# Kernel optimization log

Measured on AMD Instinct MI355X. Metric: run time of the kernel, lower is better.

Reference implementation:

```python
import jax, jax.numpy as jnp
import numpy as np

HIDDEN = 768
NUM_HEADS = 8
NUM_CELLS = 16384
MAX_HDRS = 8
NUM_HEADERS = 512
LN_EPS = 1e-5


def setup_inputs() -> dict:
    key = jax.random.key(0)
    ks = jax.random.split(key, 16)
    s = 0.02
    D = HIDDEN
    return {
        "cell_value_embeddings": jax.random.normal(ks[0], (NUM_CELLS, D), jnp.float32),
        "header_embeddings": jax.random.normal(ks[1], (NUM_HEADERS, D), jnp.float32),
        "cell_to_header_map": jax.random.randint(ks[2], (NUM_CELLS, MAX_HDRS), 0, NUM_HEADERS),
        "cell_positions": jax.random.randint(ks[3], (NUM_CELLS, 2), 0, 100),
        # nn.MultiheadAttention params
        "in_proj_w": jax.random.normal(ks[4], (3 * D, D), jnp.float32) * s,
        "in_proj_b": jnp.zeros((3 * D,), jnp.float32),
        "out_w": jax.random.normal(ks[5], (D, D), jnp.float32) * s,
        "out_b": jnp.zeros((D,), jnp.float32),
        # positional embedding tables
        "row_emb": jax.random.normal(ks[6], (100, D), jnp.float32) * s,
        "col_emb": jax.random.normal(ks[7], (100, D), jnp.float32) * s,
        # fusion: Linear(2D->D) + LayerNorm
        "fus_w": jax.random.normal(ks[8], (D, 2 * D), jnp.float32) * s,
        "fus_b": jnp.zeros((D,), jnp.float32),
        "ln_g": jnp.ones((D,), jnp.float32),
        "ln_b": jnp.zeros((D,), jnp.float32),
    }


def _forward(cell_value_embeddings, header_embeddings, in_proj_w, in_proj_b,
             out_w, out_b, row_emb, col_emb, fus_w, fus_b, ln_g, ln_b,
             cell_to_header_map, cell_positions):
    N, D = cell_value_embeddings.shape
    H = cell_to_header_map.shape[1]
    nh, dh = NUM_HEADS, D // NUM_HEADS
    scale = 1.0 / (dh ** 0.5)

    pos = jnp.clip(cell_positions, 0, 99)
    cwp = cell_value_embeddings + row_emb[pos[:, 0]] + col_emb[pos[:, 1]]  # [N,D]

    ids = cell_to_header_map
    mask = ids >= 0                                   # [N,H] valid header slots
    hg = header_embeddings[jnp.where(mask, ids, 0)]   # [N,H,D] gathered K/V inputs

    Wq, Wk, Wv = jnp.split(in_proj_w, 3, axis=0)
    bq, bk, bv = jnp.split(in_proj_b, 3)
    q = (cwp @ Wq.T + bq).reshape(N, nh, dh)          # [N,a,d]
    k = (hg @ Wk.T + bk).reshape(N, H, nh, dh)        # [N,k,a,d]
    v = (hg @ Wv.T + bv).reshape(N, H, nh, dh)

    scores = jnp.einsum('nad,nkad->nak', q, k) * scale          # [N,a,k]
    scores = jnp.where(mask[:, None, :], scores, -1e9)
    attn = jax.nn.softmax(scores, axis=-1)
    attn = jnp.where(mask[:, None, :], attn, 0.0)
    ctx = jnp.einsum('nak,nkad->nad', attn, v).reshape(N, D)
    att_out = ctx @ out_w.T + out_b                    # [N,D]

    comb = jnp.concatenate([cwp, att_out], axis=-1)    # [N,2D]
    h = comb @ fus_w.T + fus_b
    mu = jnp.mean(h, axis=-1, keepdims=True)
    var = jnp.mean((h - mu) ** 2, axis=-1, keepdims=True)
    h = (h - mu) * jax.lax.rsqrt(var + LN_EPS) * ln_g + ln_b
    fused = jax.nn.relu(h)

    has = jnp.any(mask, axis=-1)                       # cells with >=1 valid header
    enriched = jnp.where(has[:, None], fused, cwp)
    weights = jnp.where(mask, attn.mean(axis=1), 0.0)  # head-averaged attn [N,H]
    return enriched, weights


def reference(cell_value_embeddings, header_embeddings, cell_to_header_map,
              cell_positions, in_proj_w, in_proj_b, out_w, out_b, row_emb,
              col_emb, fus_w, fus_b, ln_g, ln_b):
    return _forward(cell_value_embeddings, header_embeddings, in_proj_w,
                    in_proj_b, out_w, out_b, row_emb, col_emb, fus_w, fus_b,
                    ln_g, ln_b, cell_to_header_map, cell_positions)
```

## Files before the change

### kernel.cpp

```cpp
#include <hip/hip_runtime.h>
#include <hip/hip_bf16.h>

#define NCELLS 16384
#define DIM    768
#define NHEADS 8
#define DHEAD  96
#define MAXH   8
#define ND     (NCELLS * DIM)


using bf16 = __hip_bfloat16;
typedef short  short8  __attribute__((ext_vector_type(8)));
typedef short  short4v __attribute__((ext_vector_type(4)));
typedef float  floatx4 __attribute__((ext_vector_type(4)));

__device__ inline short f2b(float f) {
    bf16 h = __float2bfloat16(f);
    unsigned short u; __builtin_memcpy(&u, &h, 2); return (short)u;
}
__device__ inline float b2f(short u) {
    unsigned x = ((unsigned)(unsigned short)u) << 16;
    float f; __builtin_memcpy(&f, &x, 4); return f;
}

__device__ inline short8 ld8(const float* p) {
    floatx4 a = *reinterpret_cast<const floatx4*>(p);
    floatx4 b = *reinterpret_cast<const floatx4*>(p + 4);
    short8 o;
#pragma unroll
    for (int i = 0; i < 4; ++i) { o[i] = f2b(a[i]); o[i + 4] = f2b(b[i]); }
    return o;
}

__device__ __forceinline__ void cp16(const void* g, void* l) {
    __builtin_amdgcn_global_load_lds(
        (const __attribute__((address_space(1))) void*)g,
        (__attribute__((address_space(3))) void*)l, 16, 0, 0);
}

template <int DUAL, int COUT>
__global__ __launch_bounds__(256) void gemm_bf(
    const bf16* __restrict__ A, const bf16* __restrict__ A2,
    const bf16* __restrict__ W, int ldw,
    const float* __restrict__ bias,
    float* __restrict__ Cf, bf16* __restrict__ Cb, int K)
{
    __shared__ short As[128 * 64];
    __shared__ short Bs[128 * 64];
    const int tid = threadIdx.x, wave = tid >> 6, lane = tid & 63;
    const int id = blockIdx.x;
    const int m0 = (id & 127) * 128;
    const int n0 = (id >> 7) * 128;
    const int wr = (wave & 1) * 64, wc = (wave >> 1) * 64;
    const int fr = lane & 15, kg = lane >> 4;

    const int srow = lane >> 3;
    const int scol = (lane & 7) ^ srow;

    floatx4 acc[16];
#pragma unroll
    for (int i = 0; i < 16; ++i) acc[i] = (floatx4){0.f, 0.f, 0.f, 0.f};

    for (int k0 = 0; k0 < K; k0 += 64) {
        const bf16* Ak; int ka;
        if (!DUAL || k0 < DIM) { Ak = A;  ka = k0; }
        else                   { Ak = A2; ka = k0 - DIM; }

        __syncthreads();
#pragma unroll
        for (int i = 0; i < 4; ++i) {
            const int c = i * 4 + wave;
            const int row = c * 8 + srow;
            cp16(Ak + (size_t)(m0 + row) * DIM + ka + scol * 8,
                 &As[c * 512 + lane * 8]);
            cp16(W  + (size_t)(n0 + row) * ldw + k0 + scol * 8,
                 &Bs[c * 512 + lane * 8]);
        }
        __syncthreads();

#pragma unroll
        for (int kk = 0; kk < 2; ++kk) {
            short8 af[4], bfv[4];
#pragma unroll
            for (int i = 0; i < 4; ++i) {
                const int sa = ((kk * 4 + kg) ^ (fr & 7)) * 8;
                af[i]  = *reinterpret_cast<const short8*>(&As[(wr + i * 16 + fr) * 64 + sa]);
                bfv[i] = *reinterpret_cast<const short8*>(&Bs[(wc + i * 16 + fr) * 64 + sa]);
            }
#pragma unroll
            for (int i = 0; i < 4; ++i)
#pragma unroll
                for (int j = 0; j < 4; ++j)
                    acc[i * 4 + j] = __builtin_amdgcn_mfma_f32_16x16x32_bf16(
                        af[i], bfv[j], acc[i * 4 + j], 0, 0, 0);
        }
    }

    const int col_l = lane & 15, row_q = kg * 4;
#pragma unroll
    for (int j = 0; j < 4; ++j) {
        const int col = n0 + wc + j * 16 + col_l;
        const float bv = bias[col];
#pragma unroll
        for (int i = 0; i < 4; ++i) {
#pragma unroll
            for (int r = 0; r < 4; ++r) {
                const int row = m0 + wr + i * 16 + row_q + r;
                const float v = acc[i * 4 + j][r] + bv;
                if (COUT == 0) Cf[(size_t)row * DIM + col] = v;
                else           Cb[(size_t)row * DIM + col] = __float2bfloat16(v);
            }
        }
    }
}

__global__ __launch_bounds__(256) void prep_kernel(
    const float* __restrict__ ce, const int* __restrict__ pos,
    const float* __restrict__ re, const float* __restrict__ co,
    bf16* __restrict__ cwp_b,
    const float* __restrict__ in_proj_w, bf16* __restrict__ Wq_b,
    const float* __restrict__ fus_w,     bf16* __restrict__ Wf_b,
    const float* __restrict__ out_w, const float* __restrict__ out_b,
    const float* __restrict__ fus_b, float* __restrict__ bco,
    const float* __restrict__ hdr, const float* __restrict__ in_proj_b,
    bf16* __restrict__ HKV)
{
    __shared__ short As[64 * 72];
    __shared__ short Bs[64 * 72];
    const int b = blockIdx.x, tid = threadIdx.x;

    if (b < 192) {
        const int m0 = (b & 7) * 64, n0 = (b >> 3) * 64;
        const float* W = in_proj_w + (size_t)DIM * DIM;
        const float* bias = in_proj_b + DIM;
        const int wave = tid >> 6, lane = tid & 63;
        const int lr = tid >> 2, lc = (tid & 3) * 16;
        const int fr = lane & 15, fk = (lane >> 4) * 8;

        floatx4 acc[4];
#pragma unroll
        for (int i = 0; i < 4; ++i) acc[i] = (floatx4){0.f, 0.f, 0.f, 0.f};

        const float* ap = hdr + (size_t)(m0 + lr) * DIM + lc;
        const float* wp = W   + (size_t)(n0 + lr) * DIM + lc;
        short8 a0 = ld8(ap), a1 = ld8(ap + 8);
        short8 w0 = ld8(wp), w1 = ld8(wp + 8);

        for (int it = 0; it < 12; ++it) {
            __syncthreads();
            *reinterpret_cast<short8*>(&As[lr * 72 + lc])     = a0;
            *reinterpret_cast<short8*>(&As[lr * 72 + lc + 8]) = a1;
            *reinterpret_cast<short8*>(&Bs[lr * 72 + lc])     = w0;
            *reinterpret_cast<short8*>(&Bs[lr * 72 + lc + 8]) = w1;
            __syncthreads();
            if (it < 11) {
                const int k0 = (it + 1) * 64;
                a0 = ld8(ap + k0); a1 = ld8(ap + k0 + 8);
                w0 = ld8(wp + k0); w1 = ld8(wp + k0 + 8);
            }
#pragma unroll
            for (int kk = 0; kk < 2; ++kk) {
                short8 af = *reinterpret_cast<const short8*>(
                    &As[(wave * 16 + fr) * 72 + kk * 32 + fk]);
#pragma unroll
                for (int t = 0; t < 4; ++t) {
                    short8 bfv = *reinterpret_cast<const short8*>(
                        &Bs[(t * 16 + fr) * 72 + kk * 32 + fk]);
                    acc[t] = __builtin_amdgcn_mfma_f32_16x16x32_bf16(af, bfv, acc[t], 0, 0, 0);
                }
            }
        }
        const int col_l = lane & 15, row_q = (lane >> 4) * 4;
#pragma unroll
        for (int t = 0; t < 4; ++t) {
            const int col = n0 + t * 16 + col_l;
            const float bv = bias[col];
#pragma unroll
            for (int r = 0; r < 4; ++r) {
                const int row = m0 + wave * 16 + row_q + r;
                HKV[(size_t)row * 1536 + col] = __float2bfloat16(acc[t][r] + bv);
            }
        }
    } else if (b < 336) {
        const int b3 = b - 192;
        const int n0  = (b3 % 12) * 64;
        const int k0t = (b3 / 12) * 64;
        const int wave = tid >> 6, lane = tid & 63;
        const int lr = tid >> 2, lc = (tid & 3) * 16;
        const int fr = lane & 15, fk = (lane >> 4) * 8;

        floatx4 acc[4];
#pragma unroll
        for (int i = 0; i < 4; ++i) acc[i] = (floatx4){0.f, 0.f, 0.f, 0.f};

        const float* ap = fus_w + (size_t)(n0 + lr) * 1536 + 768 + lc;
        const float* bp = out_w + (size_t)lr * DIM + k0t + lc;
        short8 a0 = ld8(ap), a1 = ld8(ap + 8);
        floatx4 q0 = *reinterpret_cast<const floatx4*>(bp);
        floatx4 q1 = *reinterpret_cast<const floatx4*>(bp + 4);
        floatx4 q2 = *reinterpret_cast<const floatx4*>(bp + 8);
        floatx4 q3 = *reinterpret_cast<const floatx4*>(bp + 12);

        for (int it = 0; it < 12; ++it) {
            __syncthreads();
            *reinterpret_cast<short8*>(&As[lr * 72 + lc])     = a0;
            *reinterpret_cast<short8*>(&As[lr * 72 + lc + 8]) = a1;
#pragma unroll
            for (int e = 0; e < 4; ++e) {
                Bs[(lc + e) * 72 + lr]      = f2b(q0[e]);
                Bs[(lc + 4 + e) * 72 + lr]  = f2b(q1[e]);
                Bs[(lc + 8 + e) * 72 + lr]  = f2b(q2[e]);
                Bs[(lc + 12 + e) * 72 + lr] = f2b(q3[e]);
            }
            __syncthreads();
            if (it < 11) {
                const int r0 = (it + 1) * 64;
                a0 = ld8(ap + r0); a1 = ld8(ap + r0 + 8);
                const float* bq = bp + (size_t)r0 * DIM;
                q0 = *reinterpret_cast<const floatx4*>(bq);
                q1 = *reinterpret_cast<const floatx4*>(bq + 4);
                q2 = *reinterpret_cast<const floatx4*>(bq + 8);
                q3 = *reinterpret_cast<const floatx4*>(bq + 12);
            }
#pragma unroll
            for (int kk = 0; kk < 2; ++kk) {
                short8 af = *reinterpret_cast<const short8*>(
                    &As[(wave * 16 + fr) * 72 + kk * 32 + fk]);
#pragma unroll
                for (int t = 0; t < 4; ++t) {
                    short8 bfv = *reinterpret_cast<const short8*>(
                        &Bs[(t * 16 + fr) * 72 + kk * 32 + fk]);
                    acc[t] = __builtin_amdgcn_mfma_f32_16x16x32_bf16(af, bfv, acc[t], 0, 0, 0);
                }
            }
        }
        const int col_l = lane & 15, row_q = (lane >> 4) * 4;
#pragma unroll
        for (int t = 0; t < 4; ++t) {
            const int col = k0t + t * 16 + col_l;
#pragma unroll
            for (int r = 0; r < 4; ++r) {
                const int row = n0 + wave * 16 + row_q + r;
                Wf_b[(size_t)row * 1536 + 768 + col] = __float2bfloat16(acc[t][r]);
            }
        }
    } else if (b < 339) {
        const int n = (b - 336) * 256 + tid;
        const float* wrow = fus_w + (size_t)n * 1536 + 768;
        float acc = fus_b[n];
#pragma unroll 4
        for (int m = 0; m < 768; m += 4) {
            floatx4 wv = *reinterpret_cast<const floatx4*>(wrow + m);
            floatx4 ob = *reinterpret_cast<const floatx4*>(out_b + m);
            acc += wv[0] * ob[0] + wv[1] * ob[1] + wv[2] * ob[2] + wv[3] * ob[3];
        }
        bco[n] = acc;
    } else if (b < 915) {
        const int i = (b - 339) * 256 + tid;
        floatx4 v = *reinterpret_cast<const floatx4*>(in_proj_w + (size_t)i * 4);
        short4v o;
#pragma unroll
        for (int j = 0; j < 4; ++j) o[j] = f2b(v[j]);
        *reinterpret_cast<short4v*>((short*)Wq_b + (size_t)i * 4) = o;
    } else if (b < 1491) {
        const int i  = (b - 915) * 256 + tid;
        const int e0 = i * 4;
        const int n  = e0 / 768;
        const int k  = e0 - n * 768;
        const size_t src = (size_t)n * 1536 + k;
        floatx4 v = *reinterpret_cast<const floatx4*>(fus_w + src);
        short4v o;
#pragma unroll
        for (int j = 0; j < 4; ++j) o[j] = f2b(v[j]);
        *reinterpret_cast<short4v*>((short*)Wf_b + src) = o;
    } else {
        const int gid  = (b - 1491) * 256 + tid;
        const int cell = gid / 96;
        const int off  = (gid % 96) * 8;
        int pr = pos[cell * 2 + 0]; pr = min(max(pr, 0), 99);
        int pc = pos[cell * 2 + 1]; pc = min(max(pc, 0), 99);
        const float* a = ce + (size_t)cell * DIM + off;
        const float* bb = re + (size_t)pr * DIM + off;
        const float* c = co + (size_t)pc * DIM + off;
        floatx4 a0 = *reinterpret_cast<const floatx4*>(a);
        floatx4 a1 = *reinterpret_cast<const floatx4*>(a + 4);
        floatx4 b0 = *reinterpret_cast<const floatx4*>(bb);
        floatx4 b1 = *reinterpret_cast<const floatx4*>(bb + 4);
        floatx4 c0 = *reinterpret_cast<const floatx4*>(c);
        floatx4 c1 = *reinterpret_cast<const floatx4*>(c + 4);
        short8 o;
#pragma unroll
        for (int i = 0; i < 4; ++i) {
            o[i]     = f2b(a0[i] + b0[i] + c0[i]);
            o[i + 4] = f2b(a1[i] + b1[i] + c1[i]);
        }
        *reinterpret_cast<short8*>((short*)cwp_b + (size_t)cell * DIM + off) = o;
    }
}

__global__ __launch_bounds__(256) void attn_l_kernel(
    const bf16* __restrict__ q, bf16* __restrict__ ctx,
    const bf16* __restrict__ HKV, const int* __restrict__ map,
    float* __restrict__ wout)
{
    const int h = threadIdx.x >> 7;
    const int t = threadIdx.x & 127;
    const int cell = blockIdx.x * 2 + h;

    __shared__ short Ks[2][8 * 768];
    __shared__ int   ids[2][MAXH];
    __shared__ float msk[2][MAXH];
    __shared__ float at_l[2][64];

    if (t < MAXH) {
        int id = map[(size_t)cell * MAXH + t];
        msk[h][t] = (id >= 0) ? 1.f : 0.f;
        ids[h][t] = (id >= 0) ? id : 0;
    }

    const int a = t >> 3, j = t & 7;
    short8 qv[12];
    if (t < 64) {
        const short* qp = (const short*)q + (size_t)cell * DIM + a * DHEAD;
#pragma unroll
        for (int c = 0; c < 12; ++c)
            qv[c] = *reinterpret_cast<const short8*>(qp + c * 8);
    }

#pragma unroll
    for (int s = 0; s < 6; ++s) {
        const int P  = s * 128 + t;
        const int jr = P / 96;
        const int gi = (P - jr * 96) ^ (jr & 7);
        int id = map[(size_t)cell * MAXH + jr];
        id = (id >= 0) ? id : 0;
        cp16((const short*)HKV + (size_t)id * 1536 + gi * 8, &Ks[h][P * 8]);
    }
    __syncthreads();

    short8 vv[8];
    if (t < 96) {
        const int d0 = t * 8;
#pragma unroll
        for (int jj = 0; jj < 8; ++jj)
            vv[jj] = *reinterpret_cast<const short8*>(
                (const short*)HKV + (size_t)ids[h][jj] * 1536 + DIM + d0);
    }

    if (t < 64) {
        float s0 = 0.f, s1 = 0.f, s2 = 0.f, s3 = 0.f;
#pragma unroll
        for (int cc = 0; cc < 12; cc += 4) {
            short8 kv[4];
#pragma unroll
            for (int u = 0; u < 4; ++u) {
                const int gi = (a * 12 + cc + u) ^ (j & 7);
                kv[u] = *reinterpret_cast<const short8*>(&Ks[h][(j * 96 + gi) * 8]);
            }
#pragma unroll
            for (int e = 0; e < 8; ++e) {
                s0 += b2f(qv[cc    ][e]) * b2f(kv[0][e]);
                s1 += b2f(qv[cc + 1][e]) * b2f(kv[1][e]);
                s2 += b2f(qv[cc + 2][e]) * b2f(kv[2][e]);
                s3 += b2f(qv[cc + 3][e]) * b2f(kv[3][e]);
            }
        }
        float s = ((s0 + s1) + (s2 + s3)) * 0.10206207261596577f;
        const float mk = msk[h][j];
        s = (mk != 0.f) ? s : -1e9f;
        float m = s;
        m = fmaxf(m, __shfl_xor(m, 1));
        m = fmaxf(m, __shfl_xor(m, 2));
        m = fmaxf(m, __shfl_xor(m, 4));
        float e = expf(s - m) * mk;
        float sum = e;
        sum += __shfl_xor(sum, 1);
        sum += __shfl_xor(sum, 2);
        sum += __shfl_xor(sum, 4);
        at_l[h][t] = (sum > 0.f) ? e / sum : 0.f;
    }
    __syncthreads();

    if (t < 96) {
        const int d0 = t * 8, ha = t / 12;
        float w[8];
#pragma unroll
        for (int jj = 0; jj < 8; ++jj) w[jj] = at_l[h][ha * 8 + jj];
        float acc[8];
#pragma unroll
        for (int e = 0; e < 8; ++e) acc[e] = 0.f;
#pragma unroll
        for (int jj = 0; jj < 8; ++jj)
#pragma unroll
            for (int e = 0; e < 8; ++e) acc[e] += w[jj] * b2f(vv[jj][e]);
        short8 o;
#pragma unroll
        for (int e = 0; e < 8; ++e) o[e] = f2b(acc[e]);
        *reinterpret_cast<short8*>((short*)ctx + (size_t)cell * DIM + d0) = o;
    } else if (t < 96 + MAXH) {
        const int jj = t - 96;
        float s = 0.f;
#pragma unroll
        for (int a2 = 0; a2 < NHEADS; ++a2) s += at_l[h][a2 * 8 + jj];
        wout[(size_t)cell * MAXH + jj] = s * 0.125f;
    }
}

__global__ __launch_bounds__(384) void ln_v_kernel(
    float* io, const int* __restrict__ map,
    const float* __restrict__ ce, const int* __restrict__ pos,
    const float* __restrict__ re, const float* __restrict__ co,
    const float* __restrict__ g, const float* __restrict__ b)
{
    const int h = threadIdx.x / 192;
    const int t = threadIdx.x % 192;
    const int cell = blockIdx.x * 2 + h;
    const int wave = t >> 6, lane = t & 63;
    __shared__ float ws_[2][3], wq_[2][3];
    __shared__ int hasf[2];
    if (threadIdx.x < 2) hasf[threadIdx.x] = 0;

    float* hp = io + (size_t)cell * DIM;
    floatx4 v = *reinterpret_cast<const floatx4*>(hp + t * 4);
    float s  = v[0] + v[1] + v[2] + v[3];
    float q2 = v[0]*v[0] + v[1]*v[1] + v[2]*v[2] + v[3]*v[3];
#pragma unroll
    for (int off = 32; off > 0; off >>= 1) {
        s  += __shfl_down(s, off);
        q2 += __shfl_down(q2, off);
    }
    __syncthreads();
    if (t < MAXH && map[cell * MAXH + t] >= 0) hasf[h] = 1;
    if (lane == 0) { ws_[h][wave] = s; wq_[h][wave] = q2; }
    __syncthreads();

    const float mu  = (ws_[h][0] + ws_[h][1] + ws_[h][2]) * (1.f / 768.f);
    const float var = (wq_[h][0] + wq_[h][1] + wq_[h][2]) * (1.f / 768.f) - mu * mu;
    const float inv = rsqrtf(var + 1e-5f);

    if (hasf[h]) {
        floatx4 gv = *reinterpret_cast<const floatx4*>(g + t * 4);
        floatx4 bv = *reinterpret_cast<const floatx4*>(b + t * 4);
        floatx4 o;
#pragma unroll
        for (int e = 0; e < 4; ++e)
            o[e] = fmaxf((v[e] - mu) * inv * gv[e] + bv[e], 0.f);
        *reinterpret_cast<floatx4*>(hp + t * 4) = o;
    } else {
        int pr = pos[cell * 2 + 0]; pr = min(max(pr, 0), 99);
        int pc = pos[cell * 2 + 1]; pc = min(max(pc, 0), 99);
        floatx4 a0 = *reinterpret_cast<const floatx4*>(ce + (size_t)cell * DIM + t * 4);
        floatx4 b0 = *reinterpret_cast<const floatx4*>(re + (size_t)pr * DIM + t * 4);
        floatx4 c0 = *reinterpret_cast<const floatx4*>(co + (size_t)pc * DIM + t * 4);
        floatx4 o;
#pragma unroll
        for (int e = 0; e < 4; ++e) o[e] = a0[e] + b0[e] + c0[e];
        *reinterpret_cast<floatx4*>(hp + t * 4) = o;
    }
}

extern "C" void kernel_launch(void* const* d_in, const int* in_sizes, int n_in,
                              void* d_out, int out_size, void* d_ws, size_t ws_size,
                              hipStream_t stream) {
    (void)in_sizes; (void)n_in; (void)out_size; (void)ws_size;

    const float* cell_emb  = (const float*)d_in[0];
    const float* hdr_emb   = (const float*)d_in[1];
    const int*   map       = (const int*)d_in[2];
    const int*   pos       = (const int*)d_in[3];
    const float* in_proj_w = (const float*)d_in[4];
    const float* in_proj_b = (const float*)d_in[5];
    const float* out_w     = (const float*)d_in[6];
    const float* out_b     = (const float*)d_in[7];
    const float* row_emb   = (const float*)d_in[8];
    const float* col_emb   = (const float*)d_in[9];
    const float* fus_w     = (const float*)d_in[10];
    const float* fus_b     = (const float*)d_in[11];
    const float* ln_g      = (const float*)d_in[12];
    const float* ln_b      = (const float*)d_in[13];
    float* out = (float*)d_out;

    char* ws = (char*)d_ws;
    bf16*  HKV   = (bf16*)ws;
    bf16*  ctx_b = (bf16*)(ws + 1572864);
    bf16*  cwp_b = (bf16*)(ws + 26738688);
    bf16*  Wq_b  = (bf16*)(ws + 51904512);
    float* bco   = (float*)(ws + 53084160);
    bf16*  Wf_b  = (bf16*)(ws + 54263808);
    bf16* q_b = (bf16*)d_out;

    prep_kernel<<<7635, 256, 0, stream>>>(
        cell_emb, pos, row_emb, col_emb, cwp_b,
        in_proj_w, Wq_b, fus_w, Wf_b,
        out_w, out_b, fus_b, bco,
        hdr_emb, in_proj_b, HKV);

    gemm_bf<0, 1><<<768, 256, 0, stream>>>(
        cwp_b, nullptr, Wq_b, DIM, in_proj_b, nullptr, q_b, DIM);

    attn_l_kernel<<<NCELLS / 2, 256, 0, stream>>>(q_b, ctx_b, HKV, map, out + ND);

    gemm_bf<1, 0><<<768, 256, 0, stream>>>(
        cwp_b, ctx_b, Wf_b, 1536, bco, out, nullptr, 1536);

    ln_v_kernel<<<NCELLS / 2, 384, 0, stream>>>(out, map, cell_emb, pos,
                                                row_emb, col_emb, ln_g, ln_b);
}
```

Measured before the change: 285.4 us.

## Fuse fusion GEMM with LayerNorm/ReLU epilogue into one full-row kernel

Replaces the fusion-layer GEMM and the separate LayerNorm/select kernel with one kernel. Each 512-thread block computes all 768 output columns for 64 rows in three N passes. Row sum and sum-of-squares are accumulated in shared memory during the epilogue, and normalization, ReLU or the cwp fallback are applied in place. This removes one kernel launch and a separate full pass over the output, but the grid drops to 256 large blocks and the A tile is reloaded for each N pass.

```diff
diff --git a/kernel.cpp b/kernel.cpp
--- a/kernel.cpp
+++ b/kernel.cpp
@@ -109,6 +109,146 @@
                 const float v = acc[i * 4 + j][r] + bv;
                 if (COUT == 0) Cf[(size_t)row * DIM + col] = v;
                 else           Cb[(size_t)row * DIM + col] = __float2bfloat16(v);
+            }
+        }
+    }
+}
+
+__global__ __launch_bounds__(512) void gemm_ln_kernel(
+    const bf16* __restrict__ A, const bf16* __restrict__ A2,
+    const bf16* __restrict__ W,
+    const float* __restrict__ bco, float* __restrict__ out,
+    const int* __restrict__ map,
+    const float* __restrict__ ce, const int* __restrict__ pos,
+    const float* __restrict__ re, const float* __restrict__ co,
+    const float* __restrict__ g, const float* __restrict__ b)
+{
+    __shared__ short As[8 * 512];
+    __shared__ short Bs[32 * 512];
+    __shared__ float rsum[64][4], rsq[64][4];
+    __shared__ int   hasf[64];
+
+    const int tid = threadIdx.x, wave = tid >> 6, lane = tid & 63;
+    const int m0 = blockIdx.x * 64;
+    const int wr = (wave & 1) * 32, wc = (wave >> 1) * 64;
+    const int fr = lane & 15, kg = lane >> 4;
+    const int srow = lane >> 3;
+    const int scol = (lane & 7) ^ srow;
+    const int col_l = lane & 15, rq = kg * 4;
+
+    if (tid < 256) { ((float*)rsum)[tid] = 0.f; ((float*)rsq)[tid] = 0.f; }
+    if (tid < 64) hasf[tid] = 0;
+
+    for (int nt = 0; nt < 3; ++nt) {
+        const int n0b = nt * 256;
+        floatx4 acc[8];
+#pragma unroll
+        for (int i = 0; i < 8; ++i) acc[i] = (floatx4){0.f, 0.f, 0.f, 0.f};
+
+        for (int k0 = 0; k0 < 1536; k0 += 64) {
+            const bf16* Ak; int ka;
+            if (k0 < DIM) { Ak = A;  ka = k0; }
+            else          { Ak = A2; ka = k0 - DIM; }
+
+            __syncthreads();
+            cp16(Ak + (size_t)(m0 + wave * 8 + srow) * DIM + ka + scol * 8,
+                 &As[wave * 512 + lane * 8]);
+#pragma unroll
+            for (int u = 0; u < 4; ++u) {
+                const int c2 = wave * 4 + u;
+                cp16(W + (size_t)(n0b + c2 * 8 + srow) * 1536 + k0 + scol * 8,
+                     &Bs[c2 * 512 + lane * 8]);
+            }
+            __syncthreads();
+
+#pragma unroll
+            for (int kk = 0; kk < 2; ++kk) {
+                const int sa = ((kk * 4 + kg) ^ (fr & 7)) * 8;
+                short8 af[2], bv[4];
+#pragma unroll
+                for (int i = 0; i < 2; ++i)
+                    af[i] = *reinterpret_cast<const short8*>(&As[(wr + i * 16 + fr) * 64 + sa]);
+#pragma unroll
+                for (int j = 0; j < 4; ++j)
+                    bv[j] = *reinterpret_cast<const short8*>(&Bs[(wc + j * 16 + fr) * 64 + sa]);
+#pragma unroll
+                for (int i = 0; i < 2; ++i)
+#pragma unroll
+                    for (int j = 0; j < 4; ++j)
+                        acc[i * 4 + j] = __builtin_amdgcn_mfma_f32_16x16x32_bf16(
+                            af[i], bv[j], acc[i * 4 + j], 0, 0, 0);
+            }
+        }
+
+        float bcov[4];
+#pragma unroll
+        for (int j = 0; j < 4; ++j) bcov[j] = bco[n0b + wc + j * 16 + col_l];
+#pragma unroll
+        for (int i = 0; i < 2; ++i) {
+#pragma unroll
+            for (int r = 0; r < 4; ++r) {
+                const int rowl = wr + i * 16 + rq + r;
+                float s = 0.f, q = 0.f;
+#pragma unroll
+                for (int j = 0; j < 4; ++j) {
+                    const int col = n0b + wc + j * 16 + col_l;
+                    const float v = acc[i * 4 + j][r] + bcov[j];
+                    out[(size_t)(m0 + rowl) * DIM + col] = v;
+                    s += v; q += v * v;
+                }
+#pragma unroll
+                for (int off = 1; off < 16; off <<= 1) {
+                    s += __shfl_xor(s, off);
+                    q += __shfl_xor(q, off);
+                }
+                if (col_l == 0) {
+                    rsum[rowl][wave >> 1] += s;
+                    rsq[rowl][wave >> 1]  += q;
+                }
+            }
+        }
+    }
+
+    {
+        const int row = tid >> 3, sl = tid & 7;
+        if (map[(size_t)(m0 + row) * MAXH + sl] >= 0) hasf[row] = 1;
+    }
+    __syncthreads();
+
+    {
+        const int rowl = tid >> 3, c0 = (tid & 7) * 96;
+        const int grow = m0 + rowl;
+        const float sr = rsum[rowl][0] + rsum[rowl][1] + rsum[rowl][2] + rsum[rowl][3];
+        const float qr = rsq[rowl][0] + rsq[rowl][1] + rsq[rowl][2] + rsq[rowl][3];
+        const float mu  = sr * (1.f / 768.f);
+        const float var = qr * (1.f / 768.f) - mu * mu;
+        const float inv = rsqrtf(var + 1e-5f);
+        float* hp = out + (size_t)grow * DIM + c0;
+
+        if (hasf[rowl]) {
+#pragma unroll 4
+            for (int bq = 0; bq < 24; ++bq) {
+                floatx4 hv = *reinterpret_cast<const floatx4*>(hp + bq * 4);
+                floatx4 gv = *reinterpret_cast<const floatx4*>(g + c0 + bq * 4);
+                floatx4 bv = *reinterpret_cast<const floatx4*>(b + c0 + bq * 4);
+                floatx4 o;
+#pragma unroll
+                for (int e = 0; e < 4; ++e)
+                    o[e] = fmaxf((hv[e] - mu) * inv * gv[e] + bv[e], 0.f);
+                *reinterpret_cast<floatx4*>(hp + bq * 4) = o;
+            }
+        } else {
+            int pr = pos[grow * 2 + 0]; pr = min(max(pr, 0), 99);
+            int pc = pos[grow * 2 + 1]; pc = min(max(pc, 0), 99);
+#pragma unroll 4
+            for (int bq = 0; bq < 24; ++bq) {
+                floatx4 a0 = *reinterpret_cast<const floatx4*>(ce + (size_t)grow * DIM + c0 + bq * 4);
+                floatx4 b0 = *reinterpret_cast<const floatx4*>(re + (size_t)pr * DIM + c0 + bq * 4);
+                floatx4 c1 = *reinterpret_cast<const floatx4*>(co + (size_t)pc * DIM + c0 + bq * 4);
+                floatx4 o;
+#pragma unroll
+                for (int e = 0; e < 4; ++e) o[e] = a0[e] + b0[e] + c1[e];
+                *reinterpret_cast<floatx4*>(hp + bq * 4) = o;
             }
         }
     }
@@ -406,59 +546,6 @@
     }
 }
 
-__global__ __launch_bounds__(384) void ln_v_kernel(
-    float* io, const int* __restrict__ map,
-    const float* __restrict__ ce, const int* __restrict__ pos,
-    const float* __restrict__ re, const float* __restrict__ co,
-    const float* __restrict__ g, const float* __restrict__ b)
-{
-    const int h = threadIdx.x / 192;
-    const int t = threadIdx.x % 192;
-    const int cell = blockIdx.x * 2 + h;
-    const int wave = t >> 6, lane = t & 63;
-    __shared__ float ws_[2][3], wq_[2][3];
-    __shared__ int hasf[2];
-    if (threadIdx.x < 2) hasf[threadIdx.x] = 0;
-
-    float* hp = io + (size_t)cell * DIM;
-    floatx4 v = *reinterpret_cast<const floatx4*>(hp + t * 4);
-    float s  = v[0] + v[1] + v[2] + v[3];
-    float q2 = v[0]*v[0] + v[1]*v[1] + v[2]*v[2] + v[3]*v[3];
-#pragma unroll
-    for (int off = 32; off > 0; off >>= 1) {
-        s  += __shfl_down(s, off);
-        q2 += __shfl_down(q2, off);
-    }
-    __syncthreads();
-    if (t < MAXH && map[cell * MAXH + t] >= 0) hasf[h] = 1;
-    if (lane == 0) { ws_[h][wave] = s; wq_[h][wave] = q2; }
-    __syncthreads();
-
-    const float mu  = (ws_[h][0] + ws_[h][1] + ws_[h][2]) * (1.f / 768.f);
-    const float var = (wq_[h][0] + wq_[h][1] + wq_[h][2]) * (1.f / 768.f) - mu * mu;
-    const float inv = rsqrtf(var + 1e-5f);
-
-    if (hasf[h]) {
-        floatx4 gv = *reinterpret_cast<const floatx4*>(g + t * 4);
-        floatx4 bv = *reinterpret_cast<const floatx4*>(b + t * 4);
-        floatx4 o;
-#pragma unroll
-        for (int e = 0; e < 4; ++e)
-            o[e] = fmaxf((v[e] - mu) * inv * gv[e] + bv[e], 0.f);
-        *reinterpret_cast<floatx4*>(hp + t * 4) = o;
-    } else {
-        int pr = pos[cell * 2 + 0]; pr = min(max(pr, 0), 99);
-        int pc = pos[cell * 2 + 1]; pc = min(max(pc, 0), 99);
-        floatx4 a0 = *reinterpret_cast<const floatx4*>(ce + (size_t)cell * DIM + t * 4);
-        floatx4 b0 = *reinterpret_cast<const floatx4*>(re + (size_t)pr * DIM + t * 4);
-        floatx4 c0 = *reinterpret_cast<const floatx4*>(co + (size_t)pc * DIM + t * 4);
-        floatx4 o;
-#pragma unroll
-        for (int e = 0; e < 4; ++e) o[e] = a0[e] + b0[e] + c0[e];
-        *reinterpret_cast<floatx4*>(hp + t * 4) = o;
-    }
-}
-
 extern "C" void kernel_launch(void* const* d_in, const int* in_sizes, int n_in,
                               void* d_out, int out_size, void* d_ws, size_t ws_size,
                               hipStream_t stream) {
@@ -500,9 +587,7 @@
 
     attn_l_kernel<<<NCELLS / 2, 256, 0, stream>>>(q_b, ctx_b, HKV, map, out + ND);
 
-    gemm_bf<1, 0><<<768, 256, 0, stream>>>(
-        cwp_b, ctx_b, Wf_b, 1536, bco, out, nullptr, 1536);
-
-    ln_v_kernel<<<NCELLS / 2, 384, 0, stream>>>(out, map, cell_emb, pos,
-                                                row_emb, col_emb, ln_g, ln_b);
-}
+    gemm_ln_kernel<<<256, 512, 0, stream>>>(
+        cwp_b, ctx_b, Wf_b, bco, out, map,
+        cell_emb, pos, row_emb, col_emb, ln_g, ln_b);
+}
```

Result: slower. 334.8 us (+17.3%).
